# Performance work log

Hardware: AMD Instinct MI355X
Metric: run time of the kernel (lower is better)

## Reference

```python
import jax, jax.numpy as jnp
import numpy as np

L = 4        # num decoder layers
H = 8        # heads
D = 512      # d_model
DFF = 2048   # ffn hidden
V = 8000     # target vocab
B = 16       # batch
S_ENC = 128  # encoder seq len
T = 32       # decode target_length
START, END, NULL = 1, 2, 0
NEG = -1e9
EPS = 1e-6


def sinusoid_pos(max_len, d):
    pos = np.arange(max_len)[:, None].astype(np.float32)
    i = np.arange(d)[None, :].astype(np.float32)
    ang = pos / np.power(10000.0, (2.0 * np.floor(i / 2.0)) / d)
    pe = np.where(np.arange(d)[None, :] % 2 == 0, np.sin(ang), np.cos(ang))
    return jnp.asarray(pe[None], jnp.float32)  # [1, max_len, d]


def setup_inputs() -> dict:
    key = jax.random.key(0)
    ks = jax.random.split(key, 16)
    g = lambda k, shape: jax.random.normal(k, shape, jnp.float32) * 0.02
    return {
        "target_length": T,
        "encoder_output": jax.random.normal(ks[0], (B, S_ENC, D), jnp.float32),
        "padding_mask": jnp.zeros((B, S_ENC), jnp.float32),  # 1.0 where padded
        "embed": g(ks[1], (V, D)),
        "wq": g(ks[2], (L, D, D)), "wk": g(ks[3], (L, D, D)),
        "wv": g(ks[4], (L, D, D)), "wo": g(ks[5], (L, D, D)),
        "cwq": g(ks[6], (L, D, D)), "cwk": g(ks[7], (L, D, D)),
        "cwv": g(ks[8], (L, D, D)), "cwo": g(ks[9], (L, D, D)),
        "w1": g(ks[10], (L, D, DFF)), "b1": jnp.zeros((L, DFF), jnp.float32),
        "w2": g(ks[11], (L, DFF, D)), "b2": jnp.zeros((L, D), jnp.float32),
        "ln_g": jnp.ones((L, 3, D), jnp.float32), "ln_b": jnp.zeros((L, 3, D), jnp.float32),
        "fc_w": g(ks[12], (D, V)), "fc_b": jnp.zeros((V,), jnp.float32),
    }


def ln(x, g, b):
    m = jnp.mean(x, axis=-1, keepdims=True)
    v = jnp.mean(jnp.square(x - m), axis=-1, keepdims=True)
    return (x - m) * jax.lax.rsqrt(v + EPS) * g + b


def mha(q_in, kv_in, wq, wk, wv, wo, mask):
    Bn, Sq, d = q_in.shape
    dh = d // H
    q = (q_in @ wq).reshape(Bn, Sq, H, dh)
    k = (kv_in @ wk).reshape(Bn, -1, H, dh)
    v = (kv_in @ wv).reshape(Bn, -1, H, dh)
    s = jnp.einsum('bqhd,bkhd->bhqk', q, k) / jnp.sqrt(jnp.float32(dh)) + mask
    a = jax.nn.softmax(s, axis=-1)
    o = jnp.einsum('bhqk,bkhd->bqhd', a, v).reshape(Bn, Sq, d)
    return o @ wo


def decoder_stack(x, encoder_output, self_mask, cross_mask,
                  wq, wk, wv, wo, cwq, cwk, cwv, cwo,
                  w1, b1, w2, b2, ln_g, ln_b):
    for i in range(L):
        a = mha(x, x, wq[i], wk[i], wv[i], wo[i], self_mask)
        x = ln(x + a, ln_g[i, 0], ln_b[i, 0])
        a2 = mha(x, encoder_output, cwq[i], cwk[i], cwv[i], cwo[i], cross_mask)
        x = ln(x + a2, ln_g[i, 1], ln_b[i, 1])
        f = jax.nn.relu(x @ w1[i] + b1[i]) @ w2[i] + b2[i]
        x = ln(x + f, ln_g[i, 2], ln_b[i, 2])
    return x


def reference(target_length, encoder_output, padding_mask, embed,
              wq, wk, wv, wo, cwq, cwk, cwv, cwo,
              w1, b1, w2, b2, ln_g, ln_b, fc_w, fc_b):
    Bn, S, d = encoder_output.shape
    Tp1 = target_length + 1
    pos_enc = sinusoid_pos(Tp1, d)
    sqrt_d = jnp.sqrt(jnp.float32(d))
    cross_mask = padding_mask[:, None, None, :] * NEG  # [B,1,1,S_enc]
    tokens0 = jnp.full((Bn, Tp1), NULL, jnp.int32).at[:, 0].set(START)
    done0 = jnp.zeros((Bn,), bool)

    def step(carry, t):
        tokens, done = carry
        # re-embed the whole (fixed-size, masked) prefix buffer each step
        x = embed[tokens] * sqrt_d + pos_enc
        # only positions <= t are valid keys; no look-ahead mask (matches original)
        self_mask = jnp.where(jnp.arange(Tp1) <= t, 0.0, NEG)[None, None, None, :]
        x = decoder_stack(x, encoder_output, self_mask, cross_mask,
                          wq, wk, wv, wo, cwq, cwk, cwv, cwo,
                          w1, b1, w2, b2, ln_g, ln_b)
        out = x[:, t, :] @ fc_w + fc_b  # logits at last valid position
        max_idx = jnp.argmax(out, axis=-1).astype(jnp.int32)
        done = done | (max_idx == END)
        tok = jnp.where(done, jnp.int32(NULL), max_idx)
        tokens = tokens.at[:, t + 1].set(tok)
        return (tokens, done), None

    (tokens, done), _ = jax.lax.scan(step, (tokens0, done0), jnp.arange(target_length))
    return tokens[:, 1:].astype(jnp.int64)
```

## Files before the change

kernel.cpp:

```cpp
#include <hip/hip_runtime.h>
#include <math.h>

#define L_   4
#define H_   8
#define D_   512
#define DH   64
#define DFF_ 2048
#define V_   8000
#define B_   16
#define SENC 128
#define T_   32
#define TP1  33
#define NEGV -1e9f
#define EPSV 1e-6f
#define SQRTD 22.627416997969522f
#define XSZ  ((size_t)TP1 * B_ * D_)

__global__ __launch_bounds__(256) void gemm32_k(
    const float* __restrict__ A, const float* __restrict__ W,
    const float* __restrict__ bias, float* __restrict__ C,
    int M, int N, int K, int kchunk, size_t pstride, int relu, int tmode)
{
    __shared__ __align__(16) float As[2][16][34];
    __shared__ __align__(16) float Bs[2][16][68];
    int tid = threadIdx.x;
    int tx = tid & 15, ty = tid >> 4;
    int m0 = blockIdx.y * 32, n0 = blockIdx.x * 64;
    int kbeg = blockIdx.z * kchunk;
    int niter = kchunk >> 4;
    C += (size_t)blockIdx.z * pstride;
    int am = tid >> 2, aseg = tid & 3;
    int bk = tid >> 4, bc4 = (tid & 15) * 4;
    float4 aReg = make_float4(0.f, 0.f, 0.f, 0.f), bReg;
    {
        int k0 = kbeg;
        if (tid < 128) {
            int gm = m0 + am;
            if (gm < M) aReg = *(const float4*)&A[(size_t)gm * K + k0 + aseg * 4];
        }
        bReg = *(const float4*)&W[(size_t)(k0 + bk) * N + n0 + bc4];
    }
    if (tid < 128) {
        As[0][aseg * 4 + 0][am] = aReg.x;
        As[0][aseg * 4 + 1][am] = aReg.y;
        As[0][aseg * 4 + 2][am] = aReg.z;
        As[0][aseg * 4 + 3][am] = aReg.w;
    }
    *(float4*)&Bs[0][bk][bc4] = bReg;
    __syncthreads();
    float acc[2][4] = {};
    for (int it = 0; it < niter; it++) {
        int cur = it & 1;
        if (it + 1 < niter) {
            int k0 = kbeg + (it + 1) * 16;
            if (tid < 128) {
                int gm = m0 + am;
                aReg = make_float4(0.f, 0.f, 0.f, 0.f);
                if (gm < M) aReg = *(const float4*)&A[(size_t)gm * K + k0 + aseg * 4];
            }
            bReg = *(const float4*)&W[(size_t)(k0 + bk) * N + n0 + bc4];
        }
        #pragma unroll
        for (int kk = 0; kk < 16; kk++) {
            float2 a2 = *(const float2*)&As[cur][kk][ty * 2];
            float4 b4 = *(const float4*)&Bs[cur][kk][tx * 4];
            acc[0][0] += a2.x * b4.x; acc[0][1] += a2.x * b4.y;
            acc[0][2] += a2.x * b4.z; acc[0][3] += a2.x * b4.w;
            acc[1][0] += a2.y * b4.x; acc[1][1] += a2.y * b4.y;
            acc[1][2] += a2.y * b4.z; acc[1][3] += a2.y * b4.w;
        }
        if (it + 1 < niter) {
            int nxt = 1 - cur;
            if (tid < 128) {
                As[nxt][aseg * 4 + 0][am] = aReg.x;
                As[nxt][aseg * 4 + 1][am] = aReg.y;
                As[nxt][aseg * 4 + 2][am] = aReg.z;
                As[nxt][aseg * 4 + 3][am] = aReg.w;
            }
            *(float4*)&Bs[nxt][bk][bc4] = bReg;
        }
        __syncthreads();
    }
    #pragma unroll
    for (int i = 0; i < 2; i++) {
        int gm = m0 + ty * 2 + i;
        if (gm >= M) continue;
        #pragma unroll
        for (int j = 0; j < 4; j++) {
            int gn = n0 + tx * 4 + j;
            float vv = acc[i][j];
            if (bias) vv += bias[gn];
            if (relu) vv = fmaxf(vv, 0.f);
            if (tmode == 1)
                C[(size_t)(gm >> 7) * 65536 + (size_t)gn * SENC + (gm & 127)] = vv;
            else
                C[(size_t)gm * N + gn] = vv;
        }
    }
}

__global__ __launch_bounds__(256) void gemm_qkv_k(
    const float* __restrict__ A, const float* __restrict__ W0,
    const float* __restrict__ W1, const float* __restrict__ W2,
    float* __restrict__ Cb, int M)
{
    __shared__ __align__(16) float As[2][16][34];
    __shared__ __align__(16) float Bs[2][16][68];
    int sel = blockIdx.x >> 3;
    const float* W = (sel == 0) ? W0 : ((sel == 1) ? W1 : W2);
    float* C = Cb + (size_t)sel * XSZ;
    int tid = threadIdx.x;
    int tx = tid & 15, ty = tid >> 4;
    int m0 = blockIdx.y * 32, n0 = (blockIdx.x & 7) * 64;
    int am = tid >> 2, aseg = tid & 3;
    int bk = tid >> 4, bc4 = (tid & 15) * 4;
    float4 aReg = make_float4(0.f, 0.f, 0.f, 0.f), bReg;
    {
        if (tid < 128) {
            int gm = m0 + am;
            if (gm < M) aReg = *(const float4*)&A[(size_t)gm * D_ + aseg * 4];
        }
        bReg = *(const float4*)&W[(size_t)bk * D_ + n0 + bc4];
    }
    if (tid < 128) {
        As[0][aseg * 4 + 0][am] = aReg.x;
        As[0][aseg * 4 + 1][am] = aReg.y;
        As[0][aseg * 4 + 2][am] = aReg.z;
        As[0][aseg * 4 + 3][am] = aReg.w;
    }
    *(float4*)&Bs[0][bk][bc4] = bReg;
    __syncthreads();
    float acc[2][4] = {};
    for (int it = 0; it < 32; it++) {
        int cur = it & 1;
        if (it + 1 < 32) {
            int k0 = (it + 1) * 16;
            if (tid < 128) {
                int gm = m0 + am;
                aReg = make_float4(0.f, 0.f, 0.f, 0.f);
                if (gm < M) aReg = *(const float4*)&A[(size_t)gm * D_ + k0 + aseg * 4];
            }
            bReg = *(const float4*)&W[(size_t)(k0 + bk) * D_ + n0 + bc4];
        }
        #pragma unroll
        for (int kk = 0; kk < 16; kk++) {
            float2 a2 = *(const float2*)&As[cur][kk][ty * 2];
            float4 b4 = *(const float4*)&Bs[cur][kk][tx * 4];
            acc[0][0] += a2.x * b4.x; acc[0][1] += a2.x * b4.y;
            acc[0][2] += a2.x * b4.z; acc[0][3] += a2.x * b4.w;
            acc[1][0] += a2.y * b4.x; acc[1][1] += a2.y * b4.y;
            acc[1][2] += a2.y * b4.z; acc[1][3] += a2.y * b4.w;
        }
        if (it + 1 < 32) {
            int nxt = 1 - cur;
            if (tid < 128) {
                As[nxt][aseg * 4 + 0][am] = aReg.x;
                As[nxt][aseg * 4 + 1][am] = aReg.y;
                As[nxt][aseg * 4 + 2][am] = aReg.z;
                As[nxt][aseg * 4 + 3][am] = aReg.w;
            }
            *(float4*)&Bs[nxt][bk][bc4] = bReg;
        }
        __syncthreads();
    }
    #pragma unroll
    for (int i = 0; i < 2; i++) {
        int gm = m0 + ty * 2 + i;
        if (gm >= M) continue;
        #pragma unroll
        for (int j = 0; j < 4; j++) {
            int gn = n0 + tx * 4 + j;
            if (sel == 1)
                C[(size_t)(gm & 15) * 16896 + (size_t)gn * TP1 + (gm >> 4)] =
                    acc[i][j];
            else
                C[(size_t)gm * D_ + gn] = acc[i][j];
        }
    }
}

__global__ void init_k(int* __restrict__ tokens, int* __restrict__ done,
                       float* __restrict__ cmask, const float* __restrict__ pm)
{
    int tid = threadIdx.x + blockIdx.x * 256;
    if (tid < B_ * TP1) tokens[tid] = ((tid % TP1) == 0) ? 1 : 0;
    if (tid < B_) done[tid] = 0;
    if (tid < B_ * SENC) cmask[tid] = pm[tid] * NEGV;
}

__global__ __launch_bounds__(256) void embed_k(
    const float* __restrict__ embed, const int* __restrict__ tokens,
    float* __restrict__ x)
{
    int p = blockIdx.x;
    int b = blockIdx.y;
    int tok = tokens[b * TP1 + p];
    const float* e = embed + (size_t)tok * D_;
    float* xr = x + ((size_t)p * B_ + b) * D_;
    for (int d = threadIdx.x; d < D_; d += 256) {
        float fd = (float)(2 * (d / 2)) / (float)D_;
        float ang = (float)p / powf(10000.f, fd);
        float pe = (d & 1) ? cosf(ang) : sinf(ang);
        xr[d] = e[d] * SQRTD + pe;
    }
}

__device__ __forceinline__ float block_sum(float s) {
    __shared__ float red[4];
    #pragma unroll
    for (int off = 32; off; off >>= 1) s += __shfl_xor(s, off);
    if ((threadIdx.x & 63) == 0) red[threadIdx.x >> 6] = s;
    __syncthreads();
    float tot = red[0] + red[1] + red[2] + red[3];
    __syncthreads();
    return tot;
}

__global__ __launch_bounds__(256) void attn_mega_k(
    const float* __restrict__ q, const float* __restrict__ kT,
    const float* __restrict__ v, const float* __restrict__ wo,
    const float* __restrict__ KcT, const float* __restrict__ Vc,
    const float* __restrict__ cmask, const float* __restrict__ cwq,
    const float* __restrict__ cwo, float* __restrict__ x,
    const float* __restrict__ lg, const float* __restrict__ lb, int P)
{
    int r = blockIdx.x, b = r & 15;
    int tid = threadIdx.x;
    int c0 = tid * 2;
    __shared__ float xs[D_], arow[D_];
    __shared__ float scs[H_][SENC];
    __shared__ float inv[H_];
    {
        int kp = tid & 31, h = tid >> 5;
        float acc = 0.f;
        if (kp < P) {
            const float* qr = q + (size_t)r * D_ + h * 64;
            const float* kb = kT + ((size_t)(b * 8 + h) * 64) * TP1 + kp;
            #pragma unroll 8
            for (int d = 0; d < 64; d++) acc += qr[d] * kb[(size_t)d * TP1];
        }
        scs[h][kp] = acc * 0.125f;
    }
    __syncthreads();
    if (tid < 8) {
        float mx = -1e30f;
        for (int j = 0; j < P; j++) mx = fmaxf(mx, scs[tid][j]);
        float sum = 0.f;
        for (int j = 0; j < P; j++) {
            float e = expf(scs[tid][j] - mx);
            scs[tid][j] = e;
            sum += e;
        }
        inv[tid] = 1.f / sum;
    }
    __syncthreads();
    {
        int h = c0 >> 6;
        float o0 = 0.f, o1 = 0.f;
        for (int j = 0; j < P; j++) {
            float2 vv = *(const float2*)&v[((size_t)j * B_ + b) * D_ + c0];
            float w = scs[h][j];
            o0 += w * vv.x; o1 += w * vv.y;
        }
        arow[c0]     = o0 * inv[h];
        arow[c0 + 1] = o1 * inv[h];
    }
    __syncthreads();
    {
        float2 xv = *(const float2*)&x[(size_t)r * D_ + c0];
        float v0 = xv.x, v1 = xv.y;
        #pragma unroll 8
        for (int k = 0; k < D_; k++) {
            float a = arow[k];
            float2 wv = *(const float2*)&wo[(size_t)k * D_ + c0];
            v0 += a * wv.x; v1 += a * wv.y;
        }
        float mean = block_sum(v0 + v1) * (1.f / 512.f);
        float d0 = v0 - mean, d1 = v1 - mean;
        float var = block_sum(d0 * d0 + d1 * d1) * (1.f / 512.f);
        float rs = rsqrtf(var + EPSV);
        xs[c0]     = d0 * rs * lg[c0]     + lb[c0];
        xs[c0 + 1] = d1 * rs * lg[c0 + 1] + lb[c0 + 1];
    }
    __syncthreads();
    {
        float q0 = 0.f, q1 = 0.f;
        #pragma unroll 8
        for (int k = 0; k < D_; k++) {
            float a = xs[k];
            float2 wv = *(const float2*)&cwq[(size_t)k * D_ + c0];
            q0 += a * wv.x; q1 += a * wv.y;
        }
        arow[c0] = q0; arow[c0 + 1] = q1;
    }
    __syncthreads();
    #pragma unroll
    for (int j = 0; j < 4; j++) {
        int idx = tid + j * 256;
        int h = idx >> 7, s = idx & 127;
        const float* kb = KcT + ((size_t)(b * 512 + h * 64)) * SENC + s;
        float acc = 0.f;
        #pragma unroll 8
        for (int d = 0; d < 64; d++) acc += arow[h * 64 + d] * kb[(size_t)d * SENC];
        scs[h][s] = acc * 0.125f + cmask[b * SENC + s];
    }
    __syncthreads();
    if (tid < 8) {
        float mx = -1e30f;
        for (int s = 0; s < SENC; s++) mx = fmaxf(mx, scs[tid][s]);
        float sum = 0.f;
        for (int s = 0; s < SENC; s++) {
            float e = expf(scs[tid][s] - mx);
            scs[tid][s] = e;
            sum += e;
        }
        inv[tid] = 1.f / sum;
    }
    __syncthreads();
    {
        int h = c0 >> 6;
        float o0 = 0.f, o1 = 0.f;
        for (int s = 0; s < SENC; s++) {
            float2 vv = *(const float2*)&Vc[((size_t)b * SENC + s) * D_ + c0];
            float w = scs[h][s];
            o0 += w * vv.x; o1 += w * vv.y;
        }
        arow[c0]     = o0 * inv[h];
        arow[c0 + 1] = o1 * inv[h];
    }
    __syncthreads();
    {
        float v0 = xs[c0], v1 = xs[c0 + 1];
        #pragma unroll 8
        for (int k = 0; k < D_; k++) {
            float a = arow[k];
            float2 wv = *(const float2*)&cwo[(size_t)k * D_ + c0];
            v0 += a * wv.x; v1 += a * wv.y;
        }
        float mean = block_sum(v0 + v1) * (1.f / 512.f);
        float d0 = v0 - mean, d1 = v1 - mean;
        float var = block_sum(d0 * d0 + d1 * d1) * (1.f / 512.f);
        float rs = rsqrtf(var + EPSV);
        x[(size_t)r * D_ + c0]     = d0 * rs * lg[D_ + c0]     + lb[D_ + c0];
        x[(size_t)r * D_ + c0 + 1] = d1 * rs * lg[D_ + c0 + 1] + lb[D_ + c0 + 1];
    }
}

__global__ __launch_bounds__(256) void ln_red_k(
    float* __restrict__ x, const float* __restrict__ parts, size_t pstride,
    int nparts, const float* __restrict__ bias,
    const float* __restrict__ gam, const float* __restrict__ bet)
{
    int r = blockIdx.x;
    float* xr = x + (size_t)r * D_;
    int tid = threadIdx.x;
    float v0 = xr[tid];
    float v1 = xr[tid + 256];
    for (int s = 0; s < nparts; s++) {
        const float* pr = parts + (size_t)s * pstride + (size_t)r * D_;
        v0 += pr[tid];
        v1 += pr[tid + 256];
    }
    if (bias) { v0 += bias[tid]; v1 += bias[tid + 256]; }
    float mean = block_sum(v0 + v1) * (1.f / 512.f);
    float d0 = v0 - mean, d1 = v1 - mean;
    float var = block_sum(d0 * d0 + d1 * d1) * (1.f / 512.f);
    float rs = rsqrtf(var + EPSV);
    xr[tid]       = d0 * rs * gam[tid] + bet[tid];
    xr[tid + 256] = d1 * rs * gam[tid + 256] + bet[tid + 256];
}

__global__ __launch_bounds__(256) void logits_k(
    const float* __restrict__ x, const float* __restrict__ fcw,
    const float* __restrict__ fcb, float* __restrict__ cand_v,
    int* __restrict__ cand_i, int t)
{
    __shared__ float xs[B_][D_];
    __shared__ float red[4][64][B_];
    int tid = threadIdx.x;
    for (int i = tid; i < B_ * D_; i += 256) {
        int b = i >> 9, d = i & 511;
        xs[b][d] = x[((size_t)t * B_ + b) * D_ + d];
    }
    __syncthreads();
    int lane = tid & 63, ks = tid >> 6;
    int col = blockIdx.x * 64 + lane;
    float acc[B_] = {};
    int kb = ks * 128;
    for (int k = kb; k < kb + 128; k++) {
        float w = fcw[(size_t)k * V_ + col];
        #pragma unroll
        for (int b = 0; b < B_; b++) acc[b] += xs[b][k] * w;
    }
    #pragma unroll
    for (int b = 0; b < B_; b++) red[ks][lane][b] = acc[b];
    __syncthreads();
    if (ks == 0) {
        float bias = fcb[col];
        #pragma unroll
        for (int b = 0; b < B_; b++) {
            float val = red[0][lane][b] + red[1][lane][b]
                      + red[2][lane][b] + red[3][lane][b] + bias;
            int idx = col;
            #pragma unroll
            for (int off = 32; off; off >>= 1) {
                float ov = __shfl_down(val, off);
                int oi = __shfl_down(idx, off);
                if (ov > val || (ov == val && oi < idx)) { val = ov; idx = oi; }
            }
            if (lane == 0) {
                cand_v[(size_t)b * 125 + blockIdx.x] = val;
                cand_i[(size_t)b * 125 + blockIdx.x] = idx;
            }
        }
    }
}

__global__ __launch_bounds__(128) void argmax_k(
    const float* __restrict__ cand_v, const int* __restrict__ cand_i,
    int* __restrict__ tokens, int* __restrict__ done, int t)
{
    int b = blockIdx.x;
    int tid = threadIdx.x;
    float val = -1e30f; int idx = 0x7fffffff;
    if (tid < 125) { val = cand_v[(size_t)b * 125 + tid]; idx = cand_i[(size_t)b * 125 + tid]; }
    __shared__ float sv[128];
    __shared__ int si[128];
    sv[tid] = val; si[tid] = idx;
    __syncthreads();
    for (int s = 64; s; s >>= 1) {
        if (tid < s) {
            float ov = sv[tid + s]; int oi = si[tid + s];
            if (ov > sv[tid] || (ov == sv[tid] && oi < si[tid])) {
                sv[tid] = ov; si[tid] = oi;
            }
        }
        __syncthreads();
    }
    if (tid == 0) {
        int best = si[0];
        int dn = done[b] | (best == 2 ? 1 : 0);
        done[b] = dn;
        tokens[b * TP1 + t + 1] = dn ? 0 : best;
    }
}

__global__ void writeout_k(const int* __restrict__ tokens, int* __restrict__ out)
{
    int i = threadIdx.x + blockIdx.x * 256;
    if (i < B_ * T_) {
        int b = i / T_, j = i % T_;
        out[i] = tokens[b * TP1 + j + 1];
    }
}

extern "C" void kernel_launch(void* const* d_in, const int* in_sizes, int n_in,
                              void* d_out, int out_size, void* d_ws, size_t ws_size,
                              hipStream_t stream)
{
    const float* enc   = (const float*)d_in[1];
    const float* pm    = (const float*)d_in[2];
    const float* embed = (const float*)d_in[3];
    const float* wq    = (const float*)d_in[4];
    const float* wk    = (const float*)d_in[5];
    const float* wv    = (const float*)d_in[6];
    const float* wo    = (const float*)d_in[7];
    const float* cwq   = (const float*)d_in[8];
    const float* cwk   = (const float*)d_in[9];
    const float* cwv   = (const float*)d_in[10];
    const float* cwo   = (const float*)d_in[11];
    const float* w1    = (const float*)d_in[12];
    const float* b1    = (const float*)d_in[13];
    const float* w2    = (const float*)d_in[14];
    const float* b2    = (const float*)d_in[15];
    const float* ln_g  = (const float*)d_in[16];
    const float* ln_b  = (const float*)d_in[17];
    const float* fcw   = (const float*)d_in[18];
    const float* fcb   = (const float*)d_in[19];

    float* ws = (float*)d_ws;
    size_t off = 0;
    float* x     = ws + off; off += XSZ;
    float* qkv   = ws + off; off += 3 * XSZ;
    float* parts = ws + off; off += 4 * XSZ;
    float* ffnh  = ws + off; off += (size_t)TP1 * B_ * DFF_;
    float* cand_v= ws + off; off += (size_t)B_ * 125;
    float* KcT   = ws + off; off += (size_t)L_ * B_ * SENC * D_;
    float* Vc    = ws + off; off += (size_t)L_ * B_ * SENC * D_;
    float* cmask = ws + off; off += (size_t)B_ * SENC;
    int* cand_i  = (int*)(ws + off); off += (size_t)B_ * 125;
    int* tokens  = (int*)(ws + off); off += (B_ * TP1 + 63) & ~63;
    int* done    = (int*)(ws + off); off += 64;

    init_k<<<8, 256, 0, stream>>>(tokens, done, cmask, pm);

    const size_t KVL = (size_t)B_ * SENC * D_;
    for (int l = 0; l < L_; l++) {
        gemm32_k<<<dim3(8, (B_ * SENC) / 32), 256, 0, stream>>>(
            enc, cwk + (size_t)l * D_ * D_, nullptr, KcT + l * KVL,
            B_ * SENC, D_, D_, D_, 0, 0, 1);
        gemm32_k<<<dim3(8, (B_ * SENC) / 32), 256, 0, stream>>>(
            enc, cwv + (size_t)l * D_ * D_, nullptr, Vc + l * KVL,
            B_ * SENC, D_, D_, D_, 0, 0, 0);
    }

    for (int t = 0; t < T_; t++) {
        int P = t + 1;
        int M = P * B_;
        int mt = (M + 31) / 32;

        embed_k<<<dim3(P, B_), 256, 0, stream>>>(embed, tokens, x);

        for (int l = 0; l < L_; l++) {
            const size_t lw = (size_t)l * D_ * D_;
            gemm_qkv_k<<<dim3(24, mt), 256, 0, stream>>>(
                x, wq + lw, wk + lw, wv + lw, qkv, M);
            attn_mega_k<<<M, 256, 0, stream>>>(
                qkv, qkv + XSZ, qkv + 2 * XSZ, wo + lw,
                KcT + l * KVL, Vc + l * KVL, cmask, cwq + lw, cwo + lw, x,
                ln_g + (size_t)(l * 3 + 0) * D_, ln_b + (size_t)(l * 3 + 0) * D_, P);
            gemm32_k<<<dim3(32, mt), 256, 0, stream>>>(
                x, w1 + (size_t)l * D_ * DFF_, b1 + (size_t)l * DFF_, ffnh,
                M, DFF_, D_, D_, 0, 1, 0);
            gemm32_k<<<dim3(8, mt, 4), 256, 0, stream>>>(
                ffnh, w2 + (size_t)l * DFF_ * D_, nullptr, parts,
                M, D_, DFF_, 512, XSZ, 0, 0);
            ln_red_k<<<M, 256, 0, stream>>>(x, parts, XSZ, 4, b2 + (size_t)l * D_,
                ln_g + (size_t)(l * 3 + 2) * D_, ln_b + (size_t)(l * 3 + 2) * D_);
        }

        logits_k<<<V_ / 64, 256, 0, stream>>>(x, fcw, fcb, cand_v, cand_i, t);
        argmax_k<<<B_, 128, 0, stream>>>(cand_v, cand_i, tokens, done, t);
    }

    writeout_k<<<2, 256, 0, stream>>>(tokens, (int*)d_out);
}
```

Baseline: 24.40 ms.

## Enlarge GEMM tiles to 64x64 and batch four positions per attention block

```diff
diff --git a/kernel.cpp b/kernel.cpp
--- a/kernel.cpp
+++ b/kernel.cpp
@@ -21,11 +21,11 @@
     const float* __restrict__ bias, float* __restrict__ C,
     int M, int N, int K, int kchunk, size_t pstride, int relu, int tmode)
 {
-    __shared__ __align__(16) float As[2][16][34];
+    __shared__ __align__(16) float As[2][16][68];
     __shared__ __align__(16) float Bs[2][16][68];
     int tid = threadIdx.x;
     int tx = tid & 15, ty = tid >> 4;
-    int m0 = blockIdx.y * 32, n0 = blockIdx.x * 64;
+    int m0 = blockIdx.y * 64, n0 = blockIdx.x * 64;
     int kbeg = blockIdx.z * kchunk;
     int niter = kchunk >> 4;
     C += (size_t)blockIdx.z * pstride;
@@ -33,68 +33,75 @@
     int bk = tid >> 4, bc4 = (tid & 15) * 4;
     float4 aReg = make_float4(0.f, 0.f, 0.f, 0.f), bReg;
     {
-        int k0 = kbeg;
-        if (tid < 128) {
-            int gm = m0 + am;
-            if (gm < M) aReg = *(const float4*)&A[(size_t)gm * K + k0 + aseg * 4];
-        }
-        bReg = *(const float4*)&W[(size_t)(k0 + bk) * N + n0 + bc4];
-    }
-    if (tid < 128) {
-        As[0][aseg * 4 + 0][am] = aReg.x;
-        As[0][aseg * 4 + 1][am] = aReg.y;
-        As[0][aseg * 4 + 2][am] = aReg.z;
-        As[0][aseg * 4 + 3][am] = aReg.w;
-    }
+        int gm = m0 + am;
+        if (gm < M) aReg = *(const float4*)&A[(size_t)gm * K + kbeg + aseg * 4];
+        bReg = *(const float4*)&W[(size_t)(kbeg + bk) * N + n0 + bc4];
+    }
+    As[0][aseg * 4 + 0][am] = aReg.x;
+    As[0][aseg * 4 + 1][am] = aReg.y;
+    As[0][aseg * 4 + 2][am] = aReg.z;
+    As[0][aseg * 4 + 3][am] = aReg.w;
     *(float4*)&Bs[0][bk][bc4] = bReg;
     __syncthreads();
-    float acc[2][4] = {};
+    float acc[4][4] = {};
     for (int it = 0; it < niter; it++) {
         int cur = it & 1;
         if (it + 1 < niter) {
             int k0 = kbeg + (it + 1) * 16;
-            if (tid < 128) {
-                int gm = m0 + am;
-                aReg = make_float4(0.f, 0.f, 0.f, 0.f);
-                if (gm < M) aReg = *(const float4*)&A[(size_t)gm * K + k0 + aseg * 4];
-            }
+            int gm = m0 + am;
+            aReg = make_float4(0.f, 0.f, 0.f, 0.f);
+            if (gm < M) aReg = *(const float4*)&A[(size_t)gm * K + k0 + aseg * 4];
             bReg = *(const float4*)&W[(size_t)(k0 + bk) * N + n0 + bc4];
         }
         #pragma unroll
         for (int kk = 0; kk < 16; kk++) {
-            float2 a2 = *(const float2*)&As[cur][kk][ty * 2];
+            float4 a4 = *(const float4*)&As[cur][kk][ty * 4];
             float4 b4 = *(const float4*)&Bs[cur][kk][tx * 4];
-            acc[0][0] += a2.x * b4.x; acc[0][1] += a2.x * b4.y;
-            acc[0][2] += a2.x * b4.z; acc[0][3] += a2.x * b4.w;
-            acc[1][0] += a2.y * b4.x; acc[1][1] += a2.y * b4.y;
-            acc[1][2] += a2.y * b4.z; acc[1][3] += a2.y * b4.w;
+            acc[0][0] += a4.x * b4.x; acc[0][1] += a4.x * b4.y;
+            acc[0][2] += a4.x * b4.z; acc[0][3] += a4.x * b4.w;
+            acc[1][0] += a4.y * b4.x; acc[1][1] += a4.y * b4.y;
+            acc[1][2] += a4.y * b4.z; acc[1][3] += a4.y * b4.w;
+            acc[2][0] += a4.z * b4.x; acc[2][1] += a4.z * b4.y;
+            acc[2][2] += a4.z * b4.z; acc[2][3] += a4.z * b4.w;
+            acc[3][0] += a4.w * b4.x; acc[3][1] += a4.w * b4.y;
+            acc[3][2] += a4.w * b4.z; acc[3][3] += a4.w * b4.w;
         }
         if (it + 1 < niter) {
             int nxt = 1 - cur;
-            if (tid < 128) {
-                As[nxt][aseg * 4 + 0][am] = aReg.x;
-                As[nxt][aseg * 4 + 1][am] = aReg.y;
-                As[nxt][aseg * 4 + 2][am] = aReg.z;
-                As[nxt][aseg * 4 + 3][am] = aReg.w;
-            }
+            As[nxt][aseg * 4 + 0][am] = aReg.x;
+            As[nxt][aseg * 4 + 1][am] = aReg.y;
+            As[nxt][aseg * 4 + 2][am] = aReg.z;
+            As[nxt][aseg * 4 + 3][am] = aReg.w;
             *(float4*)&Bs[nxt][bk][bc4] = bReg;
         }
         __syncthreads();
     }
     #pragma unroll
-    for (int i = 0; i < 2; i++) {
-        int gm = m0 + ty * 2 + i;
+    for (int i = 0; i < 4; i++) {
+        int gm = m0 + ty * 4 + i;
         if (gm >= M) continue;
-        #pragma unroll
-        for (int j = 0; j < 4; j++) {
-            int gn = n0 + tx * 4 + j;
-            float vv = acc[i][j];
-            if (bias) vv += bias[gn];
-            if (relu) vv = fmaxf(vv, 0.f);
-            if (tmode == 1)
+        if (tmode == 1) {
+            #pragma unroll
+            for (int j = 0; j < 4; j++) {
+                int gn = n0 + tx * 4 + j;
+                float vv = acc[i][j];
+                if (bias) vv += bias[gn];
+                if (relu) vv = fmaxf(vv, 0.f);
                 C[(size_t)(gm >> 7) * 65536 + (size_t)gn * SENC + (gm & 127)] = vv;
-            else
-                C[(size_t)gm * N + gn] = vv;
+            }
+        } else {
+            int gn = n0 + tx * 4;
+            float4 o;
+            o.x = acc[i][0]; o.y = acc[i][1]; o.z = acc[i][2]; o.w = acc[i][3];
+            if (bias) {
+                o.x += bias[gn + 0]; o.y += bias[gn + 1];
+                o.z += bias[gn + 2]; o.w += bias[gn + 3];
+            }
+            if (relu) {
+                o.x = fmaxf(o.x, 0.f); o.y = fmaxf(o.y, 0.f);
+                o.z = fmaxf(o.z, 0.f); o.w = fmaxf(o.w, 0.f);
+            }
+            *(float4*)&C[(size_t)gm * N + gn] = o;
         }
     }
 }
@@ -104,77 +111,76 @@
     const float* __restrict__ W1, const float* __restrict__ W2,
     float* __restrict__ Cb, int M)
 {
-    __shared__ __align__(16) float As[2][16][34];
+    __shared__ __align__(16) float As[2][16][68];
     __shared__ __align__(16) float Bs[2][16][68];
     int sel = blockIdx.x >> 3;
     const float* W = (sel == 0) ? W0 : ((sel == 1) ? W1 : W2);
     float* C = Cb + (size_t)sel * XSZ;
     int tid = threadIdx.x;
     int tx = tid & 15, ty = tid >> 4;
-    int m0 = blockIdx.y * 32, n0 = (blockIdx.x & 7) * 64;
+    int m0 = blockIdx.y * 64, n0 = (blockIdx.x & 7) * 64;
     int am = tid >> 2, aseg = tid & 3;
     int bk = tid >> 4, bc4 = (tid & 15) * 4;
     float4 aReg = make_float4(0.f, 0.f, 0.f, 0.f), bReg;
     {
-        if (tid < 128) {
-            int gm = m0 + am;
-            if (gm < M) aReg = *(const float4*)&A[(size_t)gm * D_ + aseg * 4];
-        }
+        int gm = m0 + am;
+        if (gm < M) aReg = *(const float4*)&A[(size_t)gm * D_ + aseg * 4];
         bReg = *(const float4*)&W[(size_t)bk * D_ + n0 + bc4];
     }
-    if (tid < 128) {
-        As[0][aseg * 4 + 0][am] = aReg.x;
-        As[0][aseg * 4 + 1][am] = aReg.y;
-        As[0][aseg * 4 + 2][am] = aReg.z;
-        As[0][aseg * 4 + 3][am] = aReg.w;
-    }
+    As[0][aseg * 4 + 0][am] = aReg.x;
+    As[0][aseg * 4 + 1][am] = aReg.y;
+    As[0][aseg * 4 + 2][am] = aReg.z;
+    As[0][aseg * 4 + 3][am] = aReg.w;
     *(float4*)&Bs[0][bk][bc4] = bReg;
     __syncthreads();
-    float acc[2][4] = {};
+    float acc[4][4] = {};
     for (int it = 0; it < 32; it++) {
         int cur = it & 1;
         if (it + 1 < 32) {
             int k0 = (it + 1) * 16;
-            if (tid < 128) {
-                int gm = m0 + am;
-                aReg = make_float4(0.f, 0.f, 0.f, 0.f);
-                if (gm < M) aReg = *(const float4*)&A[(size_t)gm * D_ + k0 + aseg * 4];
-            }
+            int gm = m0 + am;
+            aReg = make_float4(0.f, 0.f, 0.f, 0.f);
+            if (gm < M) aReg = *(const float4*)&A[(size_t)gm * D_ + k0 + aseg * 4];
             bReg = *(const float4*)&W[(size_t)(k0 + bk) * D_ + n0 + bc4];
         }
         #pragma unroll
         for (int kk = 0; kk < 16; kk++) {
-            float2 a2 = *(const float2*)&As[cur][kk][ty * 2];
+            float4 a4 = *(const float4*)&As[cur][kk][ty * 4];
             float4 b4 = *(const float4*)&Bs[cur][kk][tx * 4];
-            acc[0][0] += a2.x * b4.x; acc[0][1] += a2.x * b4.y;
-            acc[0][2] += a2.x * b4.z; acc[0][3] += a2.x * b4.w;
-            acc[1][0] += a2.y * b4.x; acc[1][1] += a2.y * b4.y;
-            acc[1][2] += a2.y * b4.z; acc[1][3] += a2.y * b4.w;
+            acc[0][0] += a4.x * b4.x; acc[0][1] += a4.x * b4.y;
+            acc[0][2] += a4.x * b4.z; acc[0][3] += a4.x * b4.w;
+            acc[1][0] += a4.y * b4.x; acc[1][1] += a4.y * b4.y;
+            acc[1][2] += a4.y * b4.z; acc[1][3] += a4.y * b4.w;
+            acc[2][0] += a4.z * b4.x; acc[2][1] += a4.z * b4.y;
+            acc[2][2] += a4.z * b4.z; acc[2][3] += a4.z * b4.w;
+            acc[3][0] += a4.w * b4.x; acc[3][1] += a4.w * b4.y;
+            acc[3][2] += a4.w * b4.z; acc[3][3] += a4.w * b4.w;
         }
         if (it + 1 < 32) {
             int nxt = 1 - cur;
-            if (tid < 128) {
-                As[nxt][aseg * 4 + 0][am] = aReg.x;
-                As[nxt][aseg * 4 + 1][am] = aReg.y;
-                As[nxt][aseg * 4 + 2][am] = aReg.z;
-                As[nxt][aseg * 4 + 3][am] = aReg.w;
-            }
+            As[nxt][aseg * 4 + 0][am] = aReg.x;
+            As[nxt][aseg * 4 + 1][am] = aReg.y;
+            As[nxt][aseg * 4 + 2][am] = aReg.z;
+            As[nxt][aseg * 4 + 3][am] = aReg.w;
             *(float4*)&Bs[nxt][bk][bc4] = bReg;
         }
         __syncthreads();
     }
     #pragma unroll
-    for (int i = 0; i < 2; i++) {
-        int gm = m0 + ty * 2 + i;
+    for (int i = 0; i < 4; i++) {
+        int gm = m0 + ty * 4 + i;
         if (gm >= M) continue;
-        #pragma unroll
-        for (int j = 0; j < 4; j++) {
-            int gn = n0 + tx * 4 + j;
-            if (sel == 1)
+        if (sel == 1) {
+            #pragma unroll
+            for (int j = 0; j < 4; j++) {
+                int gn = n0 + tx * 4 + j;
                 C[(size_t)(gm & 15) * 16896 + (size_t)gn * TP1 + (gm >> 4)] =
                     acc[i][j];
-            else
-                C[(size_t)gm * D_ + gn] = acc[i][j];
+            }
+        } else {
+            float4 o;
+            o.x = acc[i][0]; o.y = acc[i][1]; o.z = acc[i][2]; o.w = acc[i][3];
+            *(float4*)&C[(size_t)gm * D_ + n0 + tx * 4] = o;
         }
     }
 }
@@ -216,6 +222,26 @@
     return tot;
 }
 
+__device__ __forceinline__ float4 block_sum4(float4 s) {
+    __shared__ __align__(16) float red4[4][4];
+    #pragma unroll
+    for (int off = 32; off; off >>= 1) {
+        s.x += __shfl_xor(s.x, off);
+        s.y += __shfl_xor(s.y, off);
+        s.z += __shfl_xor(s.z, off);
+        s.w += __shfl_xor(s.w, off);
+    }
+    if ((threadIdx.x & 63) == 0) *(float4*)red4[threadIdx.x >> 6] = s;
+    __syncthreads();
+    float4 t;
+    t.x = red4[0][0] + red4[1][0] + red4[2][0] + red4[3][0];
+    t.y = red4[0][1] + red4[1][1] + red4[2][1] + red4[3][1];
+    t.z = red4[0][2] + red4[1][2] + red4[2][2] + red4[3][2];
+    t.w = red4[0][3] + red4[1][3] + red4[2][3] + red4[3][3];
+    __syncthreads();
+    return t;
+}
+
 __global__ __launch_bounds__(256) void attn_mega_k(
     const float* __restrict__ q, const float* __restrict__ kT,
     const float* __restrict__ v, const float* __restrict__ wo,
@@ -224,125 +250,244 @@
     const float* __restrict__ cwo, float* __restrict__ x,
     const float* __restrict__ lg, const float* __restrict__ lb, int P)
 {
-    int r = blockIdx.x, b = r & 15;
+    int b = blockIdx.x;
+    int p0 = blockIdx.y * 4;
     int tid = threadIdx.x;
     int c0 = tid * 2;
-    __shared__ float xs[D_], arow[D_];
-    __shared__ float scs[H_][SENC];
-    __shared__ float inv[H_];
-    {
-        int kp = tid & 31, h = tid >> 5;
-        float acc = 0.f;
+    __shared__ float xs[4][D_];
+    __shared__ float arow[4][D_];
+    __shared__ float scs[4][H_][SENC + 4];
+    __shared__ float inv[4][H_];
+    #pragma unroll
+    for (int g = 0; g < 4; g++) {
+        float2 qv = make_float2(0.f, 0.f);
+        if (p0 + g < P)
+            qv = *(const float2*)&q[((size_t)(p0 + g) * B_ + b) * D_ + c0];
+        *(float2*)&arow[g][c0] = qv;
+    }
+    __syncthreads();
+    {
+        int h = tid >> 5, kp = tid & 31;
+        float a0 = 0.f, a1 = 0.f, a2 = 0.f, a3 = 0.f;
         if (kp < P) {
-            const float* qr = q + (size_t)r * D_ + h * 64;
             const float* kb = kT + ((size_t)(b * 8 + h) * 64) * TP1 + kp;
             #pragma unroll 8
-            for (int d = 0; d < 64; d++) acc += qr[d] * kb[(size_t)d * TP1];
-        }
-        scs[h][kp] = acc * 0.125f;
-    }
-    __syncthreads();
-    if (tid < 8) {
+            for (int d = 0; d < 64; d++) {
+                float kv = kb[(size_t)d * TP1];
+                a0 += arow[0][h * 64 + d] * kv;
+                a1 += arow[1][h * 64 + d] * kv;
+                a2 += arow[2][h * 64 + d] * kv;
+                a3 += arow[3][h * 64 + d] * kv;
+            }
+        }
+        scs[0][h][kp] = a0 * 0.125f;
+        scs[1][h][kp] = a1 * 0.125f;
+        scs[2][h][kp] = a2 * 0.125f;
+        scs[3][h][kp] = a3 * 0.125f;
+    }
+    __syncthreads();
+    {
+        int gh = tid >> 3, lane8 = tid & 7;
+        int g = gh >> 3, h = gh & 7;
         float mx = -1e30f;
-        for (int j = 0; j < P; j++) mx = fmaxf(mx, scs[tid][j]);
+        for (int j = lane8; j < P; j += 8) mx = fmaxf(mx, scs[g][h][j]);
+        mx = fmaxf(mx, __shfl_xor(mx, 1));
+        mx = fmaxf(mx, __shfl_xor(mx, 2));
+        mx = fmaxf(mx, __shfl_xor(mx, 4));
         float sum = 0.f;
-        for (int j = 0; j < P; j++) {
-            float e = expf(scs[tid][j] - mx);
-            scs[tid][j] = e;
+        for (int j = lane8; j < P; j += 8) {
+            float e = expf(scs[g][h][j] - mx);
+            scs[g][h][j] = e;
             sum += e;
         }
-        inv[tid] = 1.f / sum;
-    }
-    __syncthreads();
-    {
-        int h = c0 >> 6;
-        float o0 = 0.f, o1 = 0.f;
+        sum += __shfl_xor(sum, 1);
+        sum += __shfl_xor(sum, 2);
+        sum += __shfl_xor(sum, 4);
+        if (lane8 == 0) inv[g][h] = 1.f / sum;
+    }
+    __syncthreads();
+    {
+        int h = tid >> 5;
+        float o0[4] = {0.f, 0.f, 0.f, 0.f}, o1[4] = {0.f, 0.f, 0.f, 0.f};
         for (int j = 0; j < P; j++) {
             float2 vv = *(const float2*)&v[((size_t)j * B_ + b) * D_ + c0];
-            float w = scs[h][j];
-            o0 += w * vv.x; o1 += w * vv.y;
-        }
-        arow[c0]     = o0 * inv[h];
-        arow[c0 + 1] = o1 * inv[h];
-    }
-    __syncthreads();
-    {
-        float2 xv = *(const float2*)&x[(size_t)r * D_ + c0];
-        float v0 = xv.x, v1 = xv.y;
+            #pragma unroll
+            for (int g = 0; g < 4; g++) {
+                float w = scs[g][h][j];
+                o0[g] += w * vv.x; o1[g] += w * vv.y;
+            }
+        }
+        #pragma unroll
+        for (int g = 0; g < 4; g++) {
+            arow[g][c0]     = o0[g] * inv[g][h];
+            arow[g][c0 + 1] = o1[g] * inv[g][h];
+        }
+    }
+    __syncthreads();
+    {
+        float v0[4], v1[4];
+        #pragma unroll
+        for (int g = 0; g < 4; g++) {
+            float2 xv = make_float2(0.f, 0.f);
+            if (p0 + g < P)
+                xv = *(const float2*)&x[((size_t)(p0 + g) * B_ + b) * D_ + c0];
+            v0[g] = xv.x; v1[g] = xv.y;
+        }
         #pragma unroll 8
         for (int k = 0; k < D_; k++) {
-            float a = arow[k];
             float2 wv = *(const float2*)&wo[(size_t)k * D_ + c0];
-            v0 += a * wv.x; v1 += a * wv.y;
-        }
-        float mean = block_sum(v0 + v1) * (1.f / 512.f);
-        float d0 = v0 - mean, d1 = v1 - mean;
-        float var = block_sum(d0 * d0 + d1 * d1) * (1.f / 512.f);
-        float rs = rsqrtf(var + EPSV);
-        xs[c0]     = d0 * rs * lg[c0]     + lb[c0];
-        xs[c0 + 1] = d1 * rs * lg[c0 + 1] + lb[c0 + 1];
-    }
-    __syncthreads();
-    {
-        float q0 = 0.f, q1 = 0.f;
+            #pragma unroll
+            for (int g = 0; g < 4; g++) {
+                float a = arow[g][k];
+                v0[g] += a * wv.x; v1[g] += a * wv.y;
+            }
+        }
+        float4 s1 = make_float4(v0[0] + v1[0], v0[1] + v1[1],
+                                v0[2] + v1[2], v0[3] + v1[3]);
+        float4 m4 = block_sum4(s1);
+        float mean[4] = {m4.x * (1.f / 512.f), m4.y * (1.f / 512.f),
+                         m4.z * (1.f / 512.f), m4.w * (1.f / 512.f)};
+        float d0[4], d1[4];
+        #pragma unroll
+        for (int g = 0; g < 4; g++) {
+            d0[g] = v0[g] - mean[g]; d1[g] = v1[g] - mean[g];
+        }
+        float4 s2 = make_float4(d0[0] * d0[0] + d1[0] * d1[0],
+                                d0[1] * d0[1] + d1[1] * d1[1],
+                                d0[2] * d0[2] + d1[2] * d1[2],
+                                d0[3] * d0[3] + d1[3] * d1[3]);
+        float4 w4 = block_sum4(s2);
+        float var[4] = {w4.x * (1.f / 512.f), w4.y * (1.f / 512.f),
+                        w4.z * (1.f / 512.f), w4.w * (1.f / 512.f)};
+        float g0 = lg[c0], g1 = lg[c0 + 1];
+        float bb0 = lb[c0], bb1 = lb[c0 + 1];
+        #pragma unroll
+        for (int g = 0; g < 4; g++) {
+            float rs = rsqrtf(var[g] + EPSV);
+            xs[g][c0]     = d0[g] * rs * g0 + bb0;
+            xs[g][c0 + 1] = d1[g] * rs * g1 + bb1;
+        }
+    }
+    __syncthreads();
+    {
+        float q0[4] = {0.f, 0.f, 0.f, 0.f}, q1[4] = {0.f, 0.f, 0.f, 0.f};
         #pragma unroll 8
         for (int k = 0; k < D_; k++) {
-            float a = xs[k];
             float2 wv = *(const float2*)&cwq[(size_t)k * D_ + c0];
-            q0 += a * wv.x; q1 += a * wv.y;
-        }
-        arow[c0] = q0; arow[c0 + 1] = q1;
+            #pragma unroll
+            for (int g = 0; g < 4; g++) {
+                float a = xs[g][k];
+                q0[g] += a * wv.x; q1[g] += a * wv.y;
+            }
+        }
+        #pragma unroll
+        for (int g = 0; g < 4; g++) {
+            arow[g][c0] = q0[g]; arow[g][c0 + 1] = q1[g];
+        }
     }
     __syncthreads();
     #pragma unroll
-    for (int j = 0; j < 4; j++) {
-        int idx = tid + j * 256;
+    for (int i = 0; i < 4; i++) {
+        int idx = tid + i * 256;
         int h = idx >> 7, s = idx & 127;
         const float* kb = KcT + ((size_t)(b * 512 + h * 64)) * SENC + s;
-        float acc = 0.f;
+        float a0 = 0.f, a1 = 0.f, a2 = 0.f, a3 = 0.f;
         #pragma unroll 8
-        for (int d = 0; d < 64; d++) acc += arow[h * 64 + d] * kb[(size_t)d * SENC];
-        scs[h][s] = acc * 0.125f + cmask[b * SENC + s];
-    }
-    __syncthreads();
-    if (tid < 8) {
+        for (int d = 0; d < 64; d++) {
+            float kc = kb[(size_t)d * SENC];
+            a0 += arow[0][h * 64 + d] * kc;
+            a1 += arow[1][h * 64 + d] * kc;
+            a2 += arow[2][h * 64 + d] * kc;
+            a3 += arow[3][h * 64 + d] * kc;
+        }
+        float cm = cmask[b * SENC + s];
+        scs[0][h][s] = a0 * 0.125f + cm;
+        scs[1][h][s] = a1 * 0.125f + cm;
+        scs[2][h][s] = a2 * 0.125f + cm;
+        scs[3][h][s] = a3 * 0.125f + cm;
+    }
+    __syncthreads();
+    {
+        int gh = tid >> 3, lane8 = tid & 7;
+        int g = gh >> 3, h = gh & 7;
         float mx = -1e30f;
-        for (int s = 0; s < SENC; s++) mx = fmaxf(mx, scs[tid][s]);
+        for (int s = lane8; s < SENC; s += 8) mx = fmaxf(mx, scs[g][h][s]);
+        mx = fmaxf(mx, __shfl_xor(mx, 1));
+        mx = fmaxf(mx, __shfl_xor(mx, 2));
+        mx = fmaxf(mx, __shfl_xor(mx, 4));
         float sum = 0.f;
-        for (int s = 0; s < SENC; s++) {
-            float e = expf(scs[tid][s] - mx);
-            scs[tid][s] = e;
+        for (int s = lane8; s < SENC; s += 8) {
+            float e = expf(scs[g][h][s] - mx);
+            scs[g][h][s] = e;
             sum += e;
         }
-        inv[tid] = 1.f / sum;
-    }
-    __syncthreads();
-    {
-        int h = c0 >> 6;
-        float o0 = 0.f, o1 = 0.f;
+        sum += __shfl_xor(sum, 1);
+        sum += __shfl_xor(sum, 2);
+        sum += __shfl_xor(sum, 4);
+        if (lane8 == 0) inv[g][h] = 1.f / sum;
+    }
+    __syncthreads();
+    {
+        int h = tid >> 5;
+        float o0[4] = {0.f, 0.f, 0.f, 0.f}, o1[4] = {0.f, 0.f, 0.f, 0.f};
         for (int s = 0; s < SENC; s++) {
             float2 vv = *(const float2*)&Vc[((size_t)b * SENC + s) * D_ + c0];
-            float w = scs[h][s];
-            o0 += w * vv.x; o1 += w * vv.y;
-        }
-        arow[c0]     = o0 * inv[h];
-        arow[c0 + 1] = o1 * inv[h];
-    }
-    __syncthreads();
-    {
-        float v0 = xs[c0], v1 = xs[c0 + 1];
+            #pragma unroll
+            for (int g = 0; g < 4; g++) {
+                float w = scs[g][h][s];
+                o0[g] += w * vv.x; o1[g] += w * vv.y;
+            }
+        }
+        #pragma unroll
+        for (int g = 0; g < 4; g++) {
+            arow[g][c0]     = o0[g] * inv[g][h];
+            arow[g][c0 + 1] = o1[g] * inv[g][h];
+        }
+    }
+    __syncthreads();
+    {
+        float v0[4], v1[4];
+        #pragma unroll
+        for (int g = 0; g < 4; g++) {
+            v0[g] = xs[g][c0]; v1[g] = xs[g][c0 + 1];
+        }
         #pragma unroll 8
         for (int k = 0; k < D_; k++) {
-            float a = arow[k];
             float2 wv = *(const float2*)&cwo[(size_t)k * D_ + c0];
-            v0 += a * wv.x; v1 += a * wv.y;
-        }
-        float mean = block_sum(v0 + v1) * (1.f / 512.f);
-        float d0 = v0 - mean, d1 = v1 - mean;
-        float var = block_sum(d0 * d0 + d1 * d1) * (1.f / 512.f);
-        float rs = rsqrtf(var + EPSV);
-        x[(size_t)r * D_ + c0]     = d0 * rs * lg[D_ + c0]     + lb[D_ + c0];
-        x[(size_t)r * D_ + c0 + 1] = d1 * rs * lg[D_ + c0 + 1] + lb[D_ + c0 + 1];
+            #pragma unroll
+            for (int g = 0; g < 4; g++) {
+                float a = arow[g][k];
+                v0[g] += a * wv.x; v1[g] += a * wv.y;
+            }
+        }
+        float4 s1 = make_float4(v0[0] + v1[0], v0[1] + v1[1],
+                                v0[2] + v1[2], v0[3] + v1[3]);
+        float4 m4 = block_sum4(s1);
+        float mean[4] = {m4.x * (1.f / 512.f), m4.y * (1.f / 512.f),
+                         m4.z * (1.f / 512.f), m4.w * (1.f / 512.f)};
+        float d0[4], d1[4];
+        #pragma unroll
+        for (int g = 0; g < 4; g++) {
+            d0[g] = v0[g] - mean[g]; d1[g] = v1[g] - mean[g];
+        }
+        float4 s2 = make_float4(d0[0] * d0[0] + d1[0] * d1[0],
+                                d0[1] * d0[1] + d1[1] * d1[1],
+                                d0[2] * d0[2] + d1[2] * d1[2],
+                                d0[3] * d0[3] + d1[3] * d1[3]);
+        float4 w4 = block_sum4(s2);
+        float var[4] = {w4.x * (1.f / 512.f), w4.y * (1.f / 512.f),
+                        w4.z * (1.f / 512.f), w4.w * (1.f / 512.f)};
+        float g0 = lg[D_ + c0], g1 = lg[D_ + c0 + 1];
+        float bb0 = lb[D_ + c0], bb1 = lb[D_ + c0 + 1];
+        #pragma unroll
+        for (int g = 0; g < 4; g++) {
+            if (p0 + g < P) {
+                float rs = rsqrtf(var[g] + EPSV);
+                float* xr = x + ((size_t)(p0 + g) * B_ + b) * D_;
+                xr[c0]     = d0[g] * rs * g0 + bb0;
+                xr[c0 + 1] = d1[g] * rs * g1 + bb1;
+            }
+        }
     }
 }
 
@@ -496,10 +641,10 @@
 
     const size_t KVL = (size_t)B_ * SENC * D_;
     for (int l = 0; l < L_; l++) {
-        gemm32_k<<<dim3(8, (B_ * SENC) / 32), 256, 0, stream>>>(
+        gemm32_k<<<dim3(8, (B_ * SENC) / 64), 256, 0, stream>>>(
             enc, cwk + (size_t)l * D_ * D_, nullptr, KcT + l * KVL,
             B_ * SENC, D_, D_, D_, 0, 0, 1);
-        gemm32_k<<<dim3(8, (B_ * SENC) / 32), 256, 0, stream>>>(
+        gemm32_k<<<dim3(8, (B_ * SENC) / 64), 256, 0, stream>>>(
             enc, cwv + (size_t)l * D_ * D_, nullptr, Vc + l * KVL,
             B_ * SENC, D_, D_, D_, 0, 0, 0);
     }
@@ -507,7 +652,7 @@
     for (int t = 0; t < T_; t++) {
         int P = t + 1;
         int M = P * B_;
-        int mt = (M + 31) / 32;
+        int mt = (M + 63) / 64;
 
         embed_k<<<dim3(P, B_), 256, 0, stream>>>(embed, tokens, x);
 
@@ -515,7 +660,7 @@
             const size_t lw = (size_t)l * D_ * D_;
             gemm_qkv_k<<<dim3(24, mt), 256, 0, stream>>>(
                 x, wq + lw, wk + lw, wv + lw, qkv, M);
-            attn_mega_k<<<M, 256, 0, stream>>>(
+            attn_mega_k<<<dim3(B_, (P + 3) / 4), 256, 0, stream>>>(
                 qkv, qkv + XSZ, qkv + 2 * XSZ, wo + lw,
                 KcT + l * KVL, Vc + l * KVL, cmask, cwq + lw, cwo + lw, x,
                 ln_g + (size_t)(l * 3 + 0) * D_, ln_b + (size_t)(l * 3 + 0) * D_, P);
```

New measurement: 25.52 ms. 4.6% more time.
